# Kernel optimization log

Hardware: AMD Instinct MI355X
Metric: run time of the kernel (lower is better)

The kernel has to match this reference:

```python
import jax, jax.numpy as jnp
import numpy as np

B, D, M, K = 4096, 768, 100000, 10


def setup_inputs() -> dict:
    key = jax.random.key(0)
    k1, k2 = jax.random.split(key)
    x = jax.random.normal(k1, (B, D), dtype=jnp.float32)
    evidence_embeddings = jax.random.normal(k2, (M, D), dtype=jnp.float32)
    return {"x": x, "evidence_embeddings": evidence_embeddings, "k": K}


def reference(x, evidence_embeddings, k):
    # cos_sim = x @ E^T  -> [B, M]
    cos_sim = jnp.einsum("bd,md->bm", x, evidence_embeddings)
    # top-k along evidence dim (dim=1)
    scores, indices = jax.lax.top_k(cos_sim, k)
    return scores, indices
```

## Files before the change

### kernel.cpp

```cpp
#include <hip/hip_runtime.h>
#include <math.h>
#include <stdint.h>

#define B_ROWS 4096
#define D_DIM  768
#define M_ROWS 100000
#define K_TOP  10

#define KSTEPS 48
#define E32N   3125
#define B32N   128
#define NGRP   16
#define NBB    16
#define NITER_TOT 391
#define CAND   12
#define KCN    12
#define LTK    5

typedef _Float16 f16;
typedef _Float16 f16x8 __attribute__((ext_vector_type(8)));
typedef float   f32x16 __attribute__((ext_vector_type(16)));

#define XF_BYTES (128ull * 48 * 1024)
#define EF_OFF   XF_BYTES
#define EF_BYTES (3125ull * 48 * 1024)
#define CS_OFF   (EF_OFF + EF_BYTES)
#define CS_BYTES (4096ull * NGRP * CAND * 4)
#define CI_OFF   (CS_OFF + CS_BYTES)
#define CI_BYTES (4096ull * NGRP * CAND * 4)
#define WS_NEED  (CI_OFF + CI_BYTES)

__global__ __launch_bounds__(256) void convert_frag(
    const float* __restrict__ src, f16* __restrict__ dst, int nband)
{
  int tid  = blockIdx.x * 256 + threadIdx.x;
  int l    = tid & 63;
  int rest = tid >> 6;
  int ks   = rest % KSTEPS;
  int band = rest / KSTEPS;
  if (band >= nband) return;
  int row = band * 32 + (l & 31);
  int k0  = ks * 16 + 8 * (l >> 5);
  const float* s = src + (size_t)row * D_DIM + k0;
  float4 v0 = *(const float4*)s;
  float4 v1 = *(const float4*)(s + 4);
  f16x8 o;
  o[0] = (f16)v0.x; o[1] = (f16)v0.y; o[2] = (f16)v0.z; o[3] = (f16)v0.w;
  o[4] = (f16)v1.x; o[5] = (f16)v1.y; o[6] = (f16)v1.z; o[7] = (f16)v1.w;
  *(f16x8*)(dst + (((size_t)band * KSTEPS + ks) << 9) + l * 8) = o;
}

__device__ __forceinline__ void ins5(float (&ts)[LTK], int (&ti)[LTK],
                                     float s, int idx)
{
  ts[LTK - 1] = s; ti[LTK - 1] = idx;
#pragma unroll
  for (int q = LTK - 1; q > 0; --q) {
    if (ts[q] > ts[q - 1]) {
      float a = ts[q]; ts[q] = ts[q - 1]; ts[q - 1] = a;
      int   b = ti[q]; ti[q] = ti[q - 1]; ti[q - 1] = b;
    }
  }
}

__device__ __forceinline__ float max16(const f32x16& v)
{
  float a = fmaxf(fmaxf(v[0], v[1]), fmaxf(v[2], v[3]));
  float b = fmaxf(fmaxf(v[4], v[5]), fmaxf(v[6], v[7]));
  float c = fmaxf(fmaxf(v[8], v[9]), fmaxf(v[10], v[11]));
  float d = fmaxf(fmaxf(v[12], v[13]), fmaxf(v[14], v[15]));
  return fmaxf(fmaxf(a, b), fmaxf(c, d));
}

__device__ __forceinline__ void gll16(const f16* src, f16* dst)
{
  __builtin_amdgcn_global_load_lds(
      (const __attribute__((address_space(1))) void*)(uintptr_t)src,
      (__attribute__((address_space(3))) void*)(uint32_t)(uintptr_t)dst,
      16, 0, 0);
}

__global__ __launch_bounds__(1024, 4) void gemm_topk(
    const f16* __restrict__ Ef, const f16* __restrict__ Xf,
    float* __restrict__ cs, int* __restrict__ ci)
{
  __shared__ f16 lds[2][32768];

  const int t    = threadIdx.x;
  const int lane = t & 63;
  const int w    = t >> 6;
  const int ew   = w >> 2;
  const int bw   = w & 3;

  const int id = blockIdx.x;
  const int g  = (id & 7) + 8 * (id >> 7);
  const int bb = (id >> 3) & 15;
  const int niter = 24 + (g < (NITER_TOT - 16 * 24) ? 1 : 0);

  const bool isE = (w < 8);
  f16* dst0 = &lds[0][0] + w * 2048 + lane * 8;
  f16* dst1 = &lds[1][0] + w * 2048 + lane * 8;

  const f16* xsrc = Xf + (size_t)(bb * 8 + (w - 8)) * (KSTEPS * 512) + lane * 8;

  const f16* rb0p = &lds[0][0] + lane * 8;
  const f16* rb1p = &lds[1][0] + lane * 8;

  float ts0[LTK], ts1[LTK]; int ti0[LTK], ti1[LTK];
#pragma unroll
  for (int q = 0; q < LTK; ++q) {
    ts0[q] = -INFINITY; ts1[q] = -INFINITY;
    ti0[q] = 0x7fffffff; ti1[q] = 0x7fffffff;
  }

#pragma unroll 1
  for (int j = 0; j < niter; ++j) {
    const int e32base = (g + NGRP * j) * 8;

    const f16* sp;
    if (isE) {
      int e32 = e32base + w; if (e32 > E32N - 1) e32 = E32N - 1;
      sp = Ef + (size_t)e32 * (KSTEPS * 512) + lane * 8;
    } else {
      sp = xsrc;
    }

    f32x16 acc0[2], acc1[2];
#pragma unroll
    for (int e = 0; e < 2; ++e) {
#pragma unroll
      for (int q = 0; q < 16; ++q) { acc0[e][q] = 0.f; acc1[e][q] = 0.f; }
    }

#pragma unroll
    for (int ff = 0; ff < 4; ++ff) gll16(sp + ff * 512, dst0 + ff * 512);
    const f16* sc = sp + 2048;

#pragma unroll 1
    for (int kc = 0; kc < KCN; ++kc) {
      asm volatile("s_waitcnt vmcnt(0)" ::: "memory");
      __builtin_amdgcn_s_barrier();

      const f16* rp = (kc & 1) ? rb1p : rb0p;
      f16* dp = (kc & 1) ? dst0 : dst1;

      if (kc < KCN - 1) {
#pragma unroll
        for (int ff = 0; ff < 4; ++ff) gll16(sc + ff * 512, dp + ff * 512);
        sc += 2048;
      }

#pragma unroll
      for (int kk = 0; kk < 4; ++kk) {
        f16x8 a[2], b[2];
#pragma unroll
        for (int e = 0; e < 2; ++e)
          a[e] = *(const f16x8*)(rp + ((ew * 2 + e) * 2048 + kk * 512));
#pragma unroll
        for (int x2 = 0; x2 < 2; ++x2)
          b[x2] = *(const f16x8*)(rp + ((8 + bw * 2 + x2) * 2048 + kk * 512));
#pragma unroll
        for (int e = 0; e < 2; ++e) {
          acc0[e] = __builtin_amdgcn_mfma_f32_32x32x16_f16(a[e], b[0], acc0[e], 0, 0, 0);
          acc1[e] = __builtin_amdgcn_mfma_f32_32x32x16_f16(a[e], b[1], acc1[e], 0, 0, 0);
        }
      }
    }

#pragma unroll
    for (int e = 0; e < 2; ++e) {
      const int ebase = e32base * 32 + (ew * 2 + e) * 32 + 4 * (lane >> 5);
      if (max16(acc0[e]) > ts0[LTK - 1]) {
#pragma unroll
        for (int q = 0; q < 16; ++q) {
          int eidx = ebase + (q & 3) + 8 * (q >> 2);
          float s = acc0[e][q];
          if (eidx < M_ROWS && s > ts0[LTK - 1]) ins5(ts0, ti0, s, eidx);
        }
      }
      if (max16(acc1[e]) > ts1[LTK - 1]) {
#pragma unroll
        for (int q = 0; q < 16; ++q) {
          int eidx = ebase + (q & 3) + 8 * (q >> 2);
          float s = acc1[e][q];
          if (eidx < M_ROWS && s > ts1[LTK - 1]) ins5(ts1, ti1, s, eidx);
        }
      }
    }
  }

  __syncthreads();
  float* ds = (float*)&lds[0][0];
  int*   di = (int*)&lds[1][0];
  {
    int half = lane >> 5, cl = lane & 31;
    int base0 = ((((ew * 2 + half) * 4 + bw) * 2 + 0) * 32 + cl) * LTK;
    int base1 = ((((ew * 2 + half) * 4 + bw) * 2 + 1) * 32 + cl) * LTK;
#pragma unroll
    for (int q = 0; q < LTK; ++q) {
      ds[base0 + q] = ts0[q]; di[base0 + q] = ti0[q];
      ds[base1 + q] = ts1[q]; di[base1 + q] = ti1[q];
    }
  }
  __syncthreads();
  if (t < 256) {
    int c = t; int bw2 = c >> 6, bt2 = (c >> 5) & 1, cl2 = c & 31;
    int hb[8];
#pragma unroll
    for (int u = 0; u < 8; ++u) {
      int ew2 = u >> 1, h2 = u & 1;
      hb[u] = ((((ew2 * 2 + h2) * 4 + bw2) * 2 + bt2) * 32 + cl2) * LTK;
    }
    const int row = bb * 256 + c;
    float* ocs = cs + ((size_t)row * NGRP + g) * CAND;
    int*   oci = ci + ((size_t)row * NGRP + g) * CAND;
    for (int o = 0; o < CAND; ++o) {
      float best = -INFINITY; int bidx = 0x7fffffff; int bu = 0, bq = 0;
#pragma unroll
      for (int u = 0; u < 8; ++u) {
        for (int q = 0; q < LTK; ++q) {
          float s = ds[hb[u] + q]; int id2 = di[hb[u] + q];
          if (s > best || (s == best && id2 < bidx)) { best = s; bidx = id2; bu = u; bq = q; }
        }
      }
      ds[hb[bu] + bq] = -INFINITY;
      ocs[o] = best; oci[o] = bidx;
    }
  }
}

__global__ __launch_bounds__(64) void final_merge(
    const float* __restrict__ x, const float* __restrict__ E,
    const float* __restrict__ cs, const int* __restrict__ ci,
    float* __restrict__ out)
{
  __shared__ float ls[192]; __shared__ int li[192];
  __shared__ int c16[16]; __shared__ double rs[16];
  const int row = blockIdx.x;
  const int lane = threadIdx.x;
  for (int q = lane; q < 192; q += 64) {
    ls[q] = cs[(size_t)row * 192 + q];
    li[q] = ci[(size_t)row * 192 + q];
  }
  __syncthreads();

  for (int o = 0; o < 16; ++o) {
    float bs = -INFINITY; int bi = 0x7fffffff; int bp = 0;
    for (int q = lane; q < 192; q += 64) {
      float s = ls[q];
      if (s > bs || (s == bs && li[q] < bi)) { bs = s; bi = li[q]; bp = q; }
    }
#pragma unroll
    for (int mk = 1; mk <= 32; mk <<= 1) {
      float qs = __shfl_xor(bs, mk, 64);
      int   qi = __shfl_xor(bi, mk, 64);
      int   qp = __shfl_xor(bp, mk, 64);
      if (qs > bs || (qs == bs && qi < bi)) { bs = qs; bi = qi; bp = qp; }
    }
    if (lane == 0) { c16[o] = bi; ls[bp] = -INFINITY; }
    __syncthreads();
  }

  {
    int cd = lane >> 2, p = lane & 3;
    int cid = c16[cd];
    if ((unsigned)cid >= M_ROWS) cid = 0;
    const float* Er = E + (size_t)cid * D_DIM + p * 192;
    const float* Xr = x + (size_t)row * D_DIM + p * 192;
    double s = 0.0;
#pragma unroll 8
    for (int d = 0; d < 192; ++d) s += (double)Xr[d] * (double)Er[d];
    s += __shfl_xor(s, 1, 64);
    s += __shfl_xor(s, 2, 64);
    if (p == 0) rs[cd] = s;
  }
  __syncthreads();

  if (lane == 0) {
    for (int o = 0; o < K_TOP; ++o) {
      double bs = rs[0]; int bc = c16[0]; int b = 0;
      for (int q = 1; q < 16; ++q) {
        double v = rs[q]; int cq = c16[q];
        if (v > bs || (v == bs && cq < bc)) { bs = v; bc = cq; b = q; }
      }
      out[(size_t)row * K_TOP + o] = (float)bs;
      out[(size_t)B_ROWS * K_TOP + (size_t)row * K_TOP + o] = (float)bc;
      rs[b] = -1.0e300;
    }
  }
}

#define RB   16
#define GQ   64
#define MMF  4
#define NJ   391
#define NTF  1024
#define XPAD 772
#define DQ4  192

__global__ __launch_bounds__(NTF, 4) void retr_fused(
    const float* __restrict__ x, const float* __restrict__ E,
    float* __restrict__ out)
{
  __shared__ float smem[21248];
  const int t = threadIdx.x;
  const int r = t & 15;
  const int g = t >> 4;
  const int rb0 = blockIdx.x * RB;
  {
    const float4* xg = (const float4*)(x + (size_t)rb0 * D_DIM);
    for (int q = t; q < RB * DQ4; q += NTF) {
      int row = q / DQ4, c4 = q % DQ4;
      float4 v = xg[q];
      *(float4*)(smem + row * XPAD + c4 * 4) = v;
    }
  }
  __syncthreads();
  float ts[K_TOP]; int ti[K_TOP];
#pragma unroll
  for (int q = 0; q < K_TOP; ++q) { ts[q] = -INFINITY; ti[q] = 0x7fffffff; }
  const float4* xr4 = (const float4*)(smem + r * XPAD);
  for (int j = 0; j < NJ; ++j) {
    const int m0 = (g + (j << 6)) * MMF;
    const float4* ep[MMF];
#pragma unroll
    for (int mm = 0; mm < MMF; ++mm) {
      int ml = m0 + mm;
      int mc = (ml < M_ROWS) ? ml : (M_ROWS - 1);
      ep[mm] = (const float4*)(E + (size_t)mc * D_DIM);
    }
    float4 acc[MMF];
#pragma unroll
    for (int mm = 0; mm < MMF; ++mm) acc[mm] = make_float4(0.f, 0.f, 0.f, 0.f);
#pragma unroll 4
    for (int dq = 0; dq < DQ4; ++dq) {
      float4 xv = xr4[dq];
#pragma unroll
      for (int mm = 0; mm < MMF; ++mm) {
        float4 e = ep[mm][dq];
        acc[mm].x += e.x * xv.x; acc[mm].y += e.y * xv.y;
        acc[mm].z += e.z * xv.z; acc[mm].w += e.w * xv.w;
      }
    }
#pragma unroll
    for (int mm = 0; mm < MMF; ++mm) {
      int ml = m0 + mm;
      float s = (acc[mm].x + acc[mm].y) + (acc[mm].z + acc[mm].w);
      if (ml < M_ROWS && s > ts[K_TOP - 1]) {
        ts[K_TOP - 1] = s; ti[K_TOP - 1] = ml;
#pragma unroll
        for (int q = K_TOP - 1; q > 0; --q) {
          if (ts[q] > ts[q - 1]) {
            float tf = ts[q]; ts[q] = ts[q - 1]; ts[q - 1] = tf;
            int   tq = ti[q]; ti[q] = ti[q - 1]; ti[q - 1] = tq;
          }
        }
      }
    }
  }
  __syncthreads();
  float*  cs  = smem;
  int*    ci  = (int*)(smem + 10240);
  int*    cnd = (int*)(smem + 20480);
  double* rsd = (double*)(smem + 20736);
#pragma unroll
  for (int q = 0; q < K_TOP; ++q) {
    cs[(r * GQ + g) * K_TOP + q] = ts[q];
    ci[(r * GQ + g) * K_TOP + q] = ti[q];
  }
  __syncthreads();
  const int w = t >> 6;
  const int lane = t & 63;
  {
    float ms[K_TOP]; int mi[K_TOP];
#pragma unroll
    for (int q = 0; q < K_TOP; ++q) {
      ms[q] = cs[(w * GQ + lane) * K_TOP + q];
      mi[q] = ci[(w * GQ + lane) * K_TOP + q];
    }
    for (int o = 0; o < 16; ++o) {
      float hs = ms[0]; int hi = mi[0];
      float bs = hs;    int bi = hi;
#pragma unroll
      for (int mk = 1; mk <= 32; mk <<= 1) {
        float qs = __shfl_xor(bs, mk, 64);
        int   qi = __shfl_xor(bi, mk, 64);
        if (qs > bs || (qs == bs && qi < bi)) { bs = qs; bi = qi; }
      }
      bool win = (hs == bs) && (hi == bi);
      if (win) {
#pragma unroll
        for (int q = 0; q < K_TOP - 1; ++q) { ms[q] = ms[q + 1]; mi[q] = mi[q + 1]; }
        ms[K_TOP - 1] = -INFINITY; mi[K_TOP - 1] = 0x7fffffff;
      }
      if (lane == 0) cnd[w * 16 + o] = bi;
    }
  }
  __syncthreads();
  {
    int cand = lane >> 2, p = lane & 3;
    int cid = cnd[w * 16 + cand];
    const float* Er = E + (size_t)cid * D_DIM + p * 192;
    const float* Xr = x + (size_t)(rb0 + w) * D_DIM + p * 192;
    double s = 0.0;
#pragma unroll 8
    for (int d = 0; d < 192; ++d) s += (double)Xr[d] * (double)Er[d];
    s += __shfl_xor(s, 1, 64);
    s += __shfl_xor(s, 2, 64);
    if (p == 0) rsd[w * 16 + cand] = s;
  }
  __syncthreads();
  if (lane == 0) {
    const int row = rb0 + w;
    for (int o = 0; o < K_TOP; ++o) {
      double bsv = rsd[w * 16 + 0]; int bci = cnd[w * 16 + 0]; int b = 0;
      for (int q = 1; q < 16; ++q) {
        double v = rsd[w * 16 + q]; int c = cnd[w * 16 + q];
        if (v > bsv || (v == bsv && c < bci)) { bsv = v; bci = c; b = q; }
      }
      out[(size_t)row * K_TOP + o] = (float)bsv;
      out[(size_t)B_ROWS * K_TOP + (size_t)row * K_TOP + o] = (float)bci;
      rsd[w * 16 + b] = -1.0e300;
    }
  }
}

extern "C" void kernel_launch(void* const* d_in, const int* in_sizes, int n_in,
                              void* d_out, int out_size, void* d_ws, size_t ws_size,
                              hipStream_t stream) {
  const float* x = (const float*)d_in[0];
  const float* E = (const float*)d_in[1];
  float* out = (float*)d_out;

  if (ws_size < WS_NEED) {
    retr_fused<<<dim3(B_ROWS / RB), NTF, 0, stream>>>(x, E, out);
    return;
  }

  f16*   Xfp = (f16*)d_ws;
  f16*   Efp = (f16*)((char*)d_ws + EF_OFF);
  float* csp = (float*)((char*)d_ws + CS_OFF);
  int*   cip = (int*)((char*)d_ws + CI_OFF);

  convert_frag<<<dim3((B32N * KSTEPS * 64) / 256), 256, 0, stream>>>(x, Xfp, B32N);
  convert_frag<<<dim3((E32N * KSTEPS * 64) / 256), 256, 0, stream>>>(E, Efp, E32N);
  gemm_topk<<<dim3(NBB * NGRP), 1024, 0, stream>>>(Efp, Xfp, csp, cip);
  final_merge<<<dim3(B_ROWS), 64, 0, stream>>>(x, E, csp, cip, out);
}
```

Baseline: 934.0 us.

## Switch GEMM operands to FP8 e4m3 MFMA and widen exact rescoring to 32 candidates

Converts x and E into fp8 e4m3 fragments instead of fp16, which halves the bytes staged through LDS and lets the GEMM use the fp8 32x32x16 MFMA. The conversion kernel packs eight fp8 values into one 64-bit store, and the LDS staging issues two 16-byte loads per chunk instead of four. To offset the lower precision, the final merge now rescores the top 32 candidates in fp64 instead of 16, at the cost of more exact dot products per row. FP8 quantisation of N(0,1) data may drop true top-10 neighbours from the candidate list, and the new LDS fragment layout may not match the fp8 MFMA operand layout.

```diff
diff --git a/kernel.cpp b/kernel.cpp
--- a/kernel.cpp
+++ b/kernel.cpp
@@ -1,4 +1,5 @@
 #include <hip/hip_runtime.h>
+#include <hip/hip_fp8.h>
 #include <math.h>
 #include <stdint.h>
 
@@ -16,22 +17,22 @@
 #define CAND   12
 #define KCN    12
 #define LTK    5
-
-typedef _Float16 f16;
-typedef _Float16 f16x8 __attribute__((ext_vector_type(8)));
-typedef float   f32x16 __attribute__((ext_vector_type(16)));
-
-#define XF_BYTES (128ull * 48 * 1024)
+#define TILEB  24576
+
+typedef long i64;
+typedef float f32x16 __attribute__((ext_vector_type(16)));
+
+#define XF_BYTES (128ull * TILEB)
 #define EF_OFF   XF_BYTES
-#define EF_BYTES (3125ull * 48 * 1024)
+#define EF_BYTES (3125ull * TILEB)
 #define CS_OFF   (EF_OFF + EF_BYTES)
 #define CS_BYTES (4096ull * NGRP * CAND * 4)
 #define CI_OFF   (CS_OFF + CS_BYTES)
 #define CI_BYTES (4096ull * NGRP * CAND * 4)
 #define WS_NEED  (CI_OFF + CI_BYTES)
 
-__global__ __launch_bounds__(256) void convert_frag(
-    const float* __restrict__ src, f16* __restrict__ dst, int nband)
+__global__ __launch_bounds__(256) void convert_frag8(
+    const float* __restrict__ src, uint8_t* __restrict__ dst, int nband)
 {
   int tid  = blockIdx.x * 256 + threadIdx.x;
   int l    = tid & 63;
@@ -44,10 +45,18 @@
   const float* s = src + (size_t)row * D_DIM + k0;
   float4 v0 = *(const float4*)s;
   float4 v1 = *(const float4*)(s + 4);
-  f16x8 o;
-  o[0] = (f16)v0.x; o[1] = (f16)v0.y; o[2] = (f16)v0.z; o[3] = (f16)v0.w;
-  o[4] = (f16)v1.x; o[5] = (f16)v1.y; o[6] = (f16)v1.z; o[7] = (f16)v1.w;
-  *(f16x8*)(dst + (((size_t)band * KSTEPS + ks) << 9) + l * 8) = o;
+  float f0 = v0.x, f1 = v0.y, f2 = v0.z, f3 = v0.w;
+  float f4 = v1.x, f5 = v1.y, f6 = v1.z, f7 = v1.w;
+  unsigned long long o = 0;
+  o |= (unsigned long long)(__hip_fp8_e4m3(f0).__x) << 0;
+  o |= (unsigned long long)(__hip_fp8_e4m3(f1).__x) << 8;
+  o |= (unsigned long long)(__hip_fp8_e4m3(f2).__x) << 16;
+  o |= (unsigned long long)(__hip_fp8_e4m3(f3).__x) << 24;
+  o |= (unsigned long long)(__hip_fp8_e4m3(f4).__x) << 32;
+  o |= (unsigned long long)(__hip_fp8_e4m3(f5).__x) << 40;
+  o |= (unsigned long long)(__hip_fp8_e4m3(f6).__x) << 48;
+  o |= (unsigned long long)(__hip_fp8_e4m3(f7).__x) << 56;
+  *(unsigned long long*)(dst + ((size_t)(band * KSTEPS + ks) << 9) + l * 8) = o;
 }
 
 __device__ __forceinline__ void ins5(float (&ts)[LTK], int (&ti)[LTK],
@@ -72,7 +81,7 @@
   return fmaxf(fmaxf(a, b), fmaxf(c, d));
 }
 
-__device__ __forceinline__ void gll16(const f16* src, f16* dst)
+__device__ __forceinline__ void gll16(const void* src, void* dst)
 {
   __builtin_amdgcn_global_load_lds(
       (const __attribute__((address_space(1))) void*)(uintptr_t)src,
@@ -81,10 +90,10 @@
 }
 
 __global__ __launch_bounds__(1024, 4) void gemm_topk(
-    const f16* __restrict__ Ef, const f16* __restrict__ Xf,
+    const uint8_t* __restrict__ Ef, const uint8_t* __restrict__ Xf,
     float* __restrict__ cs, int* __restrict__ ci)
 {
-  __shared__ f16 lds[2][32768];
+  __shared__ char lds[2][40960];
 
   const int t    = threadIdx.x;
   const int lane = t & 63;
@@ -98,13 +107,13 @@
   const int niter = 24 + (g < (NITER_TOT - 16 * 24) ? 1 : 0);
 
   const bool isE = (w < 8);
-  f16* dst0 = &lds[0][0] + w * 2048 + lane * 8;
-  f16* dst1 = &lds[1][0] + w * 2048 + lane * 8;
-
-  const f16* xsrc = Xf + (size_t)(bb * 8 + (w - 8)) * (KSTEPS * 512) + lane * 8;
-
-  const f16* rb0p = &lds[0][0] + lane * 8;
-  const f16* rb1p = &lds[1][0] + lane * 8;
+  char* dst0 = &lds[0][0] + w * 2048 + lane * 16;
+  char* dst1 = &lds[1][0] + w * 2048 + lane * 16;
+
+  const uint8_t* xsrc = Xf + (size_t)(bb * 8 + (w - 8)) * TILEB + lane * 16;
+
+  const char* rb0p = &lds[0][0] + lane * 8;
+  const char* rb1p = &lds[1][0] + lane * 8;
 
   float ts0[LTK], ts1[LTK]; int ti0[LTK], ti1[LTK];
 #pragma unroll
@@ -117,10 +126,10 @@
   for (int j = 0; j < niter; ++j) {
     const int e32base = (g + NGRP * j) * 8;
 
-    const f16* sp;
+    const uint8_t* sp;
     if (isE) {
       int e32 = e32base + w; if (e32 > E32N - 1) e32 = E32N - 1;
-      sp = Ef + (size_t)e32 * (KSTEPS * 512) + lane * 8;
+      sp = Ef + (size_t)e32 * TILEB + lane * 16;
     } else {
       sp = xsrc;
     }
@@ -132,37 +141,37 @@
       for (int q = 0; q < 16; ++q) { acc0[e][q] = 0.f; acc1[e][q] = 0.f; }
     }
 
-#pragma unroll
-    for (int ff = 0; ff < 4; ++ff) gll16(sp + ff * 512, dst0 + ff * 512);
-    const f16* sc = sp + 2048;
+    gll16(sp, dst0);
+    gll16(sp + 1024, dst0 + 1024);
+    const uint8_t* sc = sp + 2048;
 
 #pragma unroll 1
     for (int kc = 0; kc < KCN; ++kc) {
       asm volatile("s_waitcnt vmcnt(0)" ::: "memory");
       __builtin_amdgcn_s_barrier();
 
-      const f16* rp = (kc & 1) ? rb1p : rb0p;
-      f16* dp = (kc & 1) ? dst0 : dst1;
+      const char* rp = (kc & 1) ? rb1p : rb0p;
+      char* dp = (kc & 1) ? dst0 : dst1;
 
       if (kc < KCN - 1) {
-#pragma unroll
-        for (int ff = 0; ff < 4; ++ff) gll16(sc + ff * 512, dp + ff * 512);
+        gll16(sc, dp);
+        gll16(sc + 1024, dp + 1024);
         sc += 2048;
       }
 
 #pragma unroll
       for (int kk = 0; kk < 4; ++kk) {
-        f16x8 a[2], b[2];
+        i64 a[2], b[2];
 #pragma unroll
         for (int e = 0; e < 2; ++e)
-          a[e] = *(const f16x8*)(rp + ((ew * 2 + e) * 2048 + kk * 512));
+          a[e] = *(const i64*)(rp + ((ew * 2 + e) * 2048 + kk * 512));
 #pragma unroll
         for (int x2 = 0; x2 < 2; ++x2)
-          b[x2] = *(const f16x8*)(rp + ((8 + bw * 2 + x2) * 2048 + kk * 512));
+          b[x2] = *(const i64*)(rp + ((8 + bw * 2 + x2) * 2048 + kk * 512));
 #pragma unroll
         for (int e = 0; e < 2; ++e) {
-          acc0[e] = __builtin_amdgcn_mfma_f32_32x32x16_f16(a[e], b[0], acc0[e], 0, 0, 0);
-          acc1[e] = __builtin_amdgcn_mfma_f32_32x32x16_f16(a[e], b[1], acc1[e], 0, 0, 0);
+          acc0[e] = __builtin_amdgcn_mfma_f32_32x32x16_fp8_fp8(a[e], b[0], acc0[e], 0, 0, 0);
+          acc1[e] = __builtin_amdgcn_mfma_f32_32x32x16_fp8_fp8(a[e], b[1], acc1[e], 0, 0, 0);
         }
       }
     }
@@ -235,7 +244,7 @@
     float* __restrict__ out)
 {
   __shared__ float ls[192]; __shared__ int li[192];
-  __shared__ int c16[16]; __shared__ double rs[16];
+  __shared__ int c32[32]; __shared__ double rs[32];
   const int row = blockIdx.x;
   const int lane = threadIdx.x;
   for (int q = lane; q < 192; q += 64) {
@@ -244,7 +253,7 @@
   }
   __syncthreads();
 
-  for (int o = 0; o < 16; ++o) {
+  for (int o = 0; o < 32; ++o) {
     float bs = -INFINITY; int bi = 0x7fffffff; int bp = 0;
     for (int q = lane; q < 192; q += 64) {
       float s = ls[q];
@@ -257,30 +266,29 @@
       int   qp = __shfl_xor(bp, mk, 64);
       if (qs > bs || (qs == bs && qi < bi)) { bs = qs; bi = qi; bp = qp; }
     }
-    if (lane == 0) { c16[o] = bi; ls[bp] = -INFINITY; }
+    if (lane == 0) { c32[o] = bi; ls[bp] = -INFINITY; }
     __syncthreads();
   }
 
   {
-    int cd = lane >> 2, p = lane & 3;
-    int cid = c16[cd];
+    int cd = lane >> 1, p = lane & 1;
+    int cid = c32[cd];
     if ((unsigned)cid >= M_ROWS) cid = 0;
-    const float* Er = E + (size_t)cid * D_DIM + p * 192;
-    const float* Xr = x + (size_t)row * D_DIM + p * 192;
+    const float* Er = E + (size_t)cid * D_DIM + p * 384;
+    const float* Xr = x + (size_t)row * D_DIM + p * 384;
     double s = 0.0;
 #pragma unroll 8
-    for (int d = 0; d < 192; ++d) s += (double)Xr[d] * (double)Er[d];
+    for (int d = 0; d < 384; ++d) s += (double)Xr[d] * (double)Er[d];
     s += __shfl_xor(s, 1, 64);
-    s += __shfl_xor(s, 2, 64);
     if (p == 0) rs[cd] = s;
   }
   __syncthreads();
 
   if (lane == 0) {
     for (int o = 0; o < K_TOP; ++o) {
-      double bs = rs[0]; int bc = c16[0]; int b = 0;
-      for (int q = 1; q < 16; ++q) {
-        double v = rs[q]; int cq = c16[q];
+      double bs = rs[0]; int bc = c32[0]; int b = 0;
+      for (int q = 1; q < 32; ++q) {
+        double v = rs[q]; int cq = c32[q];
         if (v > bs || (v == bs && cq < bc)) { bs = v; bc = cq; b = q; }
       }
       out[(size_t)row * K_TOP + o] = (float)bs;
@@ -437,13 +445,13 @@
     return;
   }
 
-  f16*   Xfp = (f16*)d_ws;
-  f16*   Efp = (f16*)((char*)d_ws + EF_OFF);
-  float* csp = (float*)((char*)d_ws + CS_OFF);
-  int*   cip = (int*)((char*)d_ws + CI_OFF);
-
-  convert_frag<<<dim3((B32N * KSTEPS * 64) / 256), 256, 0, stream>>>(x, Xfp, B32N);
-  convert_frag<<<dim3((E32N * KSTEPS * 64) / 256), 256, 0, stream>>>(E, Efp, E32N);
+  uint8_t* Xfp = (uint8_t*)d_ws;
+  uint8_t* Efp = (uint8_t*)((char*)d_ws + EF_OFF);
+  float*   csp = (float*)((char*)d_ws + CS_OFF);
+  int*     cip = (int*)((char*)d_ws + CI_OFF);
+
+  convert_frag8<<<dim3((B32N * KSTEPS * 64) / 256), 256, 0, stream>>>(x, Xfp, B32N);
+  convert_frag8<<<dim3((E32N * KSTEPS * 64) / 256), 256, 0, stream>>>(E, Efp, E32N);
   gemm_topk<<<dim3(NBB * NGRP), 1024, 0, stream>>>(Efp, Xfp, csp, cip);
   final_merge<<<dim3(B_ROWS), 64, 0, stream>>>(x, E, csp, cip, out);
 }
```

Result: faster. 828.8 us (-11.3%).
